# Performance work log

Hardware: AMD Instinct MI355X
Metric: run time of the kernel (lower is better)

The kernel has to match this reference:

```python
import jax, jax.numpy as jnp
import numpy as np

B, C, H, W_SP = 8, 2048, 28, 28   # last_conv feature map (ResNet-50, layer4 stride=1, 448px input)
D = 8192                          # count-sketch / CBP output dim
NUM_CLS = 200
L2_EPS = 1e-12                    # F.normalize default eps


def setup_inputs() -> dict:
    key = jax.random.key(0)
    ks = jax.random.split(key, 7)
    x = jax.random.normal(ks[0], (B, C, H, W_SP), dtype=jnp.float32)
    h1 = jax.random.randint(ks[1], (C,), 0, D, dtype=jnp.int32)
    h2 = jax.random.randint(ks[2], (C,), 0, D, dtype=jnp.int32)
    # Rademacher signs (count-sketch s vectors); map {0,1} -> {-1,+1}
    s1 = (2.0 * jax.random.bernoulli(ks[3], 0.5, (C,)).astype(jnp.float32) - 1.0)
    s2 = (2.0 * jax.random.bernoulli(ks[4], 0.5, (C,)).astype(jnp.float32) - 1.0)
    W_cls = jax.random.normal(ks[5], (D, NUM_CLS), dtype=jnp.float32) * 0.01
    b_cls = jnp.zeros((NUM_CLS,), dtype=jnp.float32)
    return {"x": x, "s1": s1, "s2": s2, "W_cls": W_cls, "b_cls": b_cls, "h1": h1, "h2": h2}


def _cbp_sum(xf, s1, s2, h1, h2):
    # xf: [B, L, C] per-pixel features.  Count-sketch each pixel twice, convolve
    # via FFT, then sum over all L spatial locations (== the original HxW loop).
    Bb, L, Cc = xf.shape
    sk1 = jnp.zeros((Bb, L, D), xf.dtype).at[..., h1].add(xf * s1)  # scatter-add over channels
    sk2 = jnp.zeros((Bb, L, D), xf.dtype).at[..., h2].add(xf * s2)
    f1 = jnp.fft.rfft(sk1, axis=-1)
    f2 = jnp.fft.rfft(sk2, axis=-1)
    y = jnp.fft.irfft(f1 * f2, n=D, axis=-1)  # [B, L, D] circular conv of sketches
    return y.sum(axis=1)                      # sum over spatial locations -> [B, D]


def reference(x, s1, s2, W_cls, b_cls, h1, h2):
    Bb, Cc, Hh, Ww = x.shape
    xf = x.transpose(0, 2, 3, 1).reshape(Bb, Hh * Ww, Cc)          # [B, L, C]
    y = _cbp_sum(xf, s1, s2, h1, h2)                               # [B, D]
    feat = jnp.sign(y) * jnp.sqrt(jnp.abs(y))                      # signed sqrt
    feat = feat / jnp.maximum(jnp.linalg.norm(feat, axis=1, keepdims=True), L2_EPS)
    logit = feat @ W_cls + b_cls
    return logit, feat
```

## Files before the change

kernel.cpp:

```cpp
#include <hip/hip_runtime.h>
#include <hip/hip_bf16.h>

#define BATCH 8
#define CH    2048
#define LSP   784
#define KPAD  832
#define KSTAGE 13
#define DDIM  8192
#define NCLS  200
#define NTILE 16
#define NGRID 512
#define NUNIT 1024
#define NSLOT 64
#define FXINV (1.0f/8192.0f)

typedef _Float16 f16x8 __attribute__((ext_vector_type(8)));
typedef float    f32x4 __attribute__((ext_vector_type(4)));

#define FATOMIC(p, v) unsafeAtomicAdd((p), (v))

__global__ __launch_bounds__(256) void split_kernel(
    const float* __restrict__ x,
    _Float16* __restrict__ xh,
    float* __restrict__ part, float* __restrict__ norm,
    const float* __restrict__ s1, const int* __restrict__ h1,
    const float* __restrict__ s2, const int* __restrict__ h2,
    float4* __restrict__ metaG,
    const float* __restrict__ bc, float* __restrict__ out,
    int exclusive)
{
    int idx = blockIdx.x * 256 + threadIdx.x;
    if (!exclusive && idx < NSLOT * BATCH * DDIM / 4)
        *(float4*)&part[idx * 4] = make_float4(0.f, 0.f, 0.f, 0.f);
    if (idx < CH)
        metaG[idx] = make_float4(s1[idx] * 64.0f, __int_as_float(h1[idx]),
                                 s2[idx] * 128.0f, __int_as_float(h2[idx]));
    if (idx < BATCH) norm[idx] = 0.0f;
    if (idx < BATCH * NCLS) out[idx] = bc[idx % NCLS];
    if (idx >= BATCH * CH * KPAD / 8) return;
    int v  = idx * 8;
    int bc_ = v / KPAD;
    int l  = v - bc_ * KPAD;
    f16x8 hv = {0, 0, 0, 0, 0, 0, 0, 0};
    if (l < LSP) {
        const float* xp = &x[(size_t)bc_ * LSP + l];
        float4 a = *(const float4*)xp;
        float4 c = *(const float4*)(xp + 4);
        hv[0] = (_Float16)a.x; hv[1] = (_Float16)a.y;
        hv[2] = (_Float16)a.z; hv[3] = (_Float16)a.w;
        hv[4] = (_Float16)c.x; hv[5] = (_Float16)c.y;
        hv[6] = (_Float16)c.z; hv[7] = (_Float16)c.w;
    }
    *(f16x8*)&xh[v] = hv;
}

__device__ __forceinline__ void stage64(
    const _Float16* __restrict__ src,
    unsigned short* lds,
    int wv, int lane, int s)
{
    const int rowi = lane >> 3;
    const int gc   = (lane & 7) ^ rowi;
    const _Float16* g0 = src + (size_t)rowi * KPAD + s * 64 + gc * 8;
#pragma unroll
    for (int q = 0; q < 4; ++q) {
        const int r0 = wv * 32 + q * 8;
        __builtin_amdgcn_global_load_lds(
            (__attribute__((address_space(1))) void*)(g0 + (size_t)r0 * KPAD),
            (__attribute__((address_space(3))) void*)(lds + r0 * 64),
            16, 0, 0);
    }
}

__global__ __launch_bounds__(256, 2) void gram_scatter_kernel(
    const _Float16* __restrict__ xh,
    const float4* __restrict__ metaG,
    float* __restrict__ part,
    int exclusive)
{
    __shared__ __align__(16) unsigned short smA[128 * 64];
    __shared__ __align__(16) unsigned short smB[128 * 64];
    __shared__ __align__(16) int bins[DDIM];

    const int tid  = threadIdx.x;
    const int lane = tid & 63;
    const int wv   = tid >> 6;
    const int bid  = blockIdx.x;
    const int b    = bid & 7;

    for (int i = tid; i < DDIM; i += 256) bins[i] = 0;

    const int wrow = (wv >> 1) * 64;
    const int wcol = (wv & 1) * 64;
    const int rsel = lane & 15;
    const int khi  = lane >> 4;

#pragma unroll 1
    for (int jj = 0; jj < 2; ++jj) {
        const int unit = bid + jj * NGRID;
        int npair, tMs[2], tNs[2];
        if (unit < 64) {
            const int t2 = (unit >> 3) * 2;
            npair = 2;
            tMs[0] = tNs[0] = t2;
            tMs[1] = tNs[1] = t2 + 1;
        } else {
            npair = 1;
            int i = (unit - 64) >> 3;
            int tM = 0, tN = 0;
#pragma unroll 1
            for (int t = 0; t < NTILE - 1; ++t) {
                int c = NTILE - 1 - t;
                if (i < c) { tM = t; tN = t + 1 + i; break; }
                i -= c;
            }
            tMs[0] = tM; tNs[0] = tN;
        }

#pragma unroll 1
        for (int pp = 0; pp < npair; ++pp) {
            const int tM = tMs[pp], tN = tNs[pp];
            const bool diag = (tM == tN);

            const _Float16* srcA = xh + ((size_t)b * CH + (size_t)tM * 128) * KPAD;
            const _Float16* srcB = xh + ((size_t)b * CH + (size_t)tN * 128) * KPAD;
            const unsigned short* fragB = diag ? smA : smB;

            f32x4 acc[4][4];
            const f32x4 zv = {0.0f, 0.0f, 0.0f, 0.0f};
#pragma unroll
            for (int mi = 0; mi < 4; ++mi)
#pragma unroll
                for (int ni = 0; ni < 4; ++ni) acc[mi][ni] = zv;

#pragma unroll 1
            for (int s = 0; s < KSTAGE; ++s) {
                stage64(srcA, smA, wv, lane, s);
                if (!diag) stage64(srcB, smB, wv, lane, s);
                __syncthreads();
#pragma unroll
                for (int t = 0; t < 2; ++t) {
                    const int co = ((((t << 2) + khi) ^ (rsel & 7)) << 3);
                    f16x8 ah[4], bh[4];
#pragma unroll
                    for (int i = 0; i < 4; ++i) {
                        ah[i] = *(const f16x8*)&smA[(wrow + i * 16 + rsel) * 64 + co];
                        bh[i] = *(const f16x8*)&fragB[(wcol + i * 16 + rsel) * 64 + co];
                    }
#pragma unroll
                    for (int mi = 0; mi < 4; ++mi)
#pragma unroll
                        for (int ni = 0; ni < 4; ++ni)
                            acc[mi][ni] = __builtin_amdgcn_mfma_f32_16x16x32_f16(
                                ah[mi], bh[ni], acc[mi][ni], 0, 0, 0);
                }
                __syncthreads();
            }

            const int c2b = tN * 128 + wcol + rsel;
            int   h1c[4], h2c[4]; float s1c[4], s2c[4];
#pragma unroll
            for (int ni = 0; ni < 4; ++ni) {
                float4 cm = metaG[c2b + ni * 16];
                s1c[ni] = cm.x; h1c[ni] = __float_as_int(cm.y);
                s2c[ni] = cm.z; h2c[ni] = __float_as_int(cm.w);
            }

            const int rowbase = tM * 128 + wrow + (khi << 2);
#pragma unroll
            for (int mi = 0; mi < 4; ++mi) {
                float4 rm[4];
#pragma unroll
                for (int r = 0; r < 4; ++r) rm[r] = metaG[rowbase + mi * 16 + r];
#pragma unroll
                for (int r = 0; r < 4; ++r) {
                    const float s1r = rm[r].x, s2r = rm[r].z;
                    const int h1r = __float_as_int(rm[r].y);
                    const int h2r = __float_as_int(rm[r].w);
#pragma unroll
                    for (int ni = 0; ni < 4; ++ni) {
                        float g = acc[mi][ni][r];
                        atomicAdd(&bins[(h1r + h2c[ni]) & (DDIM - 1)],
                                  (int)(s1r * s2c[ni] * g));
                        if (!diag)
                            atomicAdd(&bins[(h1c[ni] + h2r) & (DDIM - 1)],
                                      (int)(s1c[ni] * s2r * g));
                    }
                }
            }
        }
    }

    __syncthreads();

    if (exclusive) {
        float* pbase = part + ((size_t)((bid >> 3) * BATCH + b) * DDIM);
#pragma unroll 4
        for (int i = tid; i < DDIM / 4; i += 256) {
            int4 v = *(const int4*)&bins[i * 4];
            float4 f = make_float4((float)v.x * FXINV, (float)v.y * FXINV,
                                   (float)v.z * FXINV, (float)v.w * FXINV);
            *(float4*)&pbase[i * 4] = f;
        }
    } else {
        float* pbase = part + ((size_t)((bid >> 3) * BATCH + b) * DDIM);
        const int rot = (bid & 31) << 8;
        for (int i = tid; i < DDIM; i += 256) {
            int j = (i + rot) & (DDIM - 1);
            int v = bins[j];
            if (v != 0) FATOMIC(&pbase[j], (float)v * FXINV);
        }
    }
}

__global__ __launch_bounds__(256) void reduce_kernel(
    const float* __restrict__ part, float* __restrict__ y,
    float* __restrict__ norm)
{
    const int tid = threadIdx.x;
    const int b   = blockIdx.x & 7;
    const int d0  = (blockIdx.x >> 3) * 256 + tid;
    float s = 0.0f;
#pragma unroll 8
    for (int p = 0; p < NSLOT; ++p)
        s += part[((size_t)p * BATCH + b) * DDIM + d0];
    y[(size_t)b * DDIM + d0] = s;
    float ab = fabsf(s);
    __shared__ float red[256];
    red[tid] = ab;
    __syncthreads();
    for (int st = 128; st > 0; st >>= 1) {
        if (tid < st) red[tid] += red[tid + st];
        __syncthreads();
    }
    if (tid == 0) FATOMIC(&norm[b], red[0]);
}

__global__ __launch_bounds__(256) void logit_kernel(
    const float* __restrict__ y, const float* __restrict__ norm,
    const float* __restrict__ W, float* __restrict__ out)
{
    const int j = blockIdx.x;
    const int tid = threadIdx.x;
    __shared__ float fs[BATCH][64];
    __shared__ float inv[BATCH];
    if (tid < BATCH) inv[tid] = 1.0f / fmaxf(sqrtf(norm[tid]), 1e-12f);
    __syncthreads();
    for (int i = tid; i < BATCH * 64; i += 256) {
        int bb = i >> 6, dd = i & 63;
        float v = y[(size_t)bb * DDIM + j * 64 + dd];
        float f = copysignf(sqrtf(fabsf(v)), v) * inv[bb];
        fs[bb][dd] = f;
        out[BATCH * NCLS + (size_t)bb * DDIM + j * 64 + dd] = f;
    }
    __syncthreads();
    if (tid < NCLS) {
        float a[BATCH];
#pragma unroll
        for (int bb = 0; bb < BATCH; ++bb) a[bb] = 0.0f;
        for (int dd = 0; dd < 64; ++dd) {
            float w = W[(size_t)(j * 64 + dd) * NCLS + tid];
#pragma unroll
            for (int bb = 0; bb < BATCH; ++bb) a[bb] += fs[bb][dd] * w;
        }
#pragma unroll
        for (int bb = 0; bb < BATCH; ++bb)
            FATOMIC(&out[bb * NCLS + tid], a[bb]);
    }
}

extern "C" void kernel_launch(void* const* d_in, const int* in_sizes, int n_in,
                              void* d_out, int out_size, void* d_ws, size_t ws_size,
                              hipStream_t stream)
{
    const float* x  = (const float*)d_in[0];
    const float* s1 = (const float*)d_in[1];
    const float* s2 = (const float*)d_in[2];
    const float* W  = (const float*)d_in[3];
    const float* bc = (const float*)d_in[4];
    const int*   h1 = (const int*)d_in[5];
    const int*   h2 = (const int*)d_in[6];
    float* out = (float*)d_out;

    const size_t ybytes  = (size_t)BATCH * DDIM * sizeof(float);
    const size_t xhbytes = (size_t)BATCH * CH * KPAD * sizeof(_Float16);
    const size_t partbytes = (size_t)NSLOT * BATCH * DDIM * sizeof(float);

    const int exclusive = (ws_size >= partbytes + ybytes + 128 + xhbytes);

    char* ws = (char*)d_ws;
    float* part = (float*)ws;
    float* y    = (float*)(ws + partbytes);
    float4* metaG = (float4*)(ws + partbytes);
    float* norm = (float*)(ws + partbytes + ybytes);
    _Float16* xh = (_Float16*)(ws + partbytes + ybytes + 128);

    split_kernel<<<(BATCH * CH * KPAD / 8 + 255) / 256, 256, 0, stream>>>(
        x, xh, part, norm, s1, h1, s2, h2, metaG, bc, out, exclusive);

    gram_scatter_kernel<<<NGRID, 256, 0, stream>>>(
        xh, metaG, part, exclusive);

    reduce_kernel<<<256, 256, 0, stream>>>(part, y, norm);

    logit_kernel<<<128, 256, 0, stream>>>(y, norm, W, out);
}
```

Measured before the change: 162.1 us.

## Double-buffer gram tile staging and halve grid to four units per block

The Gram-matrix kernel now double-buffers the LDS A/B tiles. It prefetches the next K-stage, or the first stage of the next tile pair, with async global-to-LDS loads and uses a partial vmcnt wait instead of full syncthreads. The grid is halved so each block processes four units, and the partial-sum slot count shrinks to match. The goal is to hide global load latency behind MFMA work and cut the number of partial buffers to reduce. The cost is doubled LDS per block (occupancy likely drops to one block per CU, and the launch-bounds occupancy hint is removed) and fewer blocks to spread across CUs.

```diff
diff --git a/kernel.cpp b/kernel.cpp
--- a/kernel.cpp
+++ b/kernel.cpp
@@ -9,9 +9,9 @@
 #define DDIM  8192
 #define NCLS  200
 #define NTILE 16
-#define NGRID 512
+#define NGRID 256
 #define NUNIT 1024
-#define NSLOT 64
+#define NSLOT 32
 #define FXINV (1.0f/8192.0f)
 
 typedef _Float16 f16x8 __attribute__((ext_vector_type(8)));
@@ -72,14 +72,14 @@
     }
 }
 
-__global__ __launch_bounds__(256, 2) void gram_scatter_kernel(
+__global__ __launch_bounds__(256) void gram_scatter_kernel(
     const _Float16* __restrict__ xh,
     const float4* __restrict__ metaG,
     float* __restrict__ part,
     int exclusive)
 {
-    __shared__ __align__(16) unsigned short smA[128 * 64];
-    __shared__ __align__(16) unsigned short smB[128 * 64];
+    __shared__ __align__(16) unsigned short smA[2][128 * 64];
+    __shared__ __align__(16) unsigned short smB[2][128 * 64];
     __shared__ __align__(16) int bins[DDIM];
 
     const int tid  = threadIdx.x;
@@ -90,22 +90,15 @@
 
     for (int i = tid; i < DDIM; i += 256) bins[i] = 0;
 
-    const int wrow = (wv >> 1) * 64;
-    const int wcol = (wv & 1) * 64;
-    const int rsel = lane & 15;
-    const int khi  = lane >> 4;
-
+    int npairs = 0, tMl[5], tNl[5];
 #pragma unroll 1
-    for (int jj = 0; jj < 2; ++jj) {
+    for (int jj = 0; jj < 4; ++jj) {
         const int unit = bid + jj * NGRID;
-        int npair, tMs[2], tNs[2];
         if (unit < 64) {
             const int t2 = (unit >> 3) * 2;
-            npair = 2;
-            tMs[0] = tNs[0] = t2;
-            tMs[1] = tNs[1] = t2 + 1;
+            tMl[npairs] = tNl[npairs] = t2;     ++npairs;
+            tMl[npairs] = tNl[npairs] = t2 + 1; ++npairs;
         } else {
-            npair = 1;
             int i = (unit - 64) >> 3;
             int tM = 0, tN = 0;
 #pragma unroll 1
@@ -114,78 +107,116 @@
                 if (i < c) { tM = t; tN = t + 1 + i; break; }
                 i -= c;
             }
-            tMs[0] = tM; tNs[0] = tN;
-        }
+            tMl[npairs] = tM; tNl[npairs] = tN; ++npairs;
+        }
+    }
+
+    const int wrow = (wv >> 1) * 64;
+    const int wcol = (wv & 1) * 64;
+    const int rsel = lane & 15;
+    const int khi  = lane >> 4;
+
+    {
+        const _Float16* a0 = xh + ((size_t)b * CH + (size_t)tMl[0] * 128) * KPAD;
+        stage64(a0, smA[0], wv, lane, 0);
+        if (tMl[0] != tNl[0]) {
+            const _Float16* b0 = xh + ((size_t)b * CH + (size_t)tNl[0] * 128) * KPAD;
+            stage64(b0, smB[0], wv, lane, 0);
+        }
+    }
+
+    int g = 0;
 
 #pragma unroll 1
-        for (int pp = 0; pp < npair; ++pp) {
-            const int tM = tMs[pp], tN = tNs[pp];
-            const bool diag = (tM == tN);
-
-            const _Float16* srcA = xh + ((size_t)b * CH + (size_t)tM * 128) * KPAD;
-            const _Float16* srcB = xh + ((size_t)b * CH + (size_t)tN * 128) * KPAD;
-            const unsigned short* fragB = diag ? smA : smB;
-
-            f32x4 acc[4][4];
-            const f32x4 zv = {0.0f, 0.0f, 0.0f, 0.0f};
-#pragma unroll
-            for (int mi = 0; mi < 4; ++mi)
-#pragma unroll
-                for (int ni = 0; ni < 4; ++ni) acc[mi][ni] = zv;
+    for (int p = 0; p < npairs; ++p) {
+        const int tM = tMl[p], tN = tNl[p];
+        const bool diag = (tM == tN);
+
+        const _Float16* srcA = xh + ((size_t)b * CH + (size_t)tM * 128) * KPAD;
+        const _Float16* srcB = xh + ((size_t)b * CH + (size_t)tN * 128) * KPAD;
+
+        f32x4 acc[4][4];
+        const f32x4 zv = {0.0f, 0.0f, 0.0f, 0.0f};
+#pragma unroll
+        for (int mi = 0; mi < 4; ++mi)
+#pragma unroll
+            for (int ni = 0; ni < 4; ++ni) acc[mi][ni] = zv;
 
 #pragma unroll 1
-            for (int s = 0; s < KSTAGE; ++s) {
-                stage64(srcA, smA, wv, lane, s);
-                if (!diag) stage64(srcB, smB, wv, lane, s);
-                __syncthreads();
-#pragma unroll
-                for (int t = 0; t < 2; ++t) {
-                    const int co = ((((t << 2) + khi) ^ (rsel & 7)) << 3);
-                    f16x8 ah[4], bh[4];
-#pragma unroll
-                    for (int i = 0; i < 4; ++i) {
-                        ah[i] = *(const f16x8*)&smA[(wrow + i * 16 + rsel) * 64 + co];
-                        bh[i] = *(const f16x8*)&fragB[(wcol + i * 16 + rsel) * 64 + co];
-                    }
-#pragma unroll
-                    for (int mi = 0; mi < 4; ++mi)
-#pragma unroll
-                        for (int ni = 0; ni < 4; ++ni)
-                            acc[mi][ni] = __builtin_amdgcn_mfma_f32_16x16x32_f16(
-                                ah[mi], bh[ni], acc[mi][ni], 0, 0, 0);
+        for (int s = 0; s < KSTAGE; ++s) {
+            const int curb = g & 1, nxtb = curb ^ 1;
+            int k = 0;
+            if (s + 1 < KSTAGE) {
+                stage64(srcA, smA[nxtb], wv, lane, s + 1);
+                if (!diag) { stage64(srcB, smB[nxtb], wv, lane, s + 1); k = 8; }
+                else k = 4;
+            } else if (p + 1 < npairs) {
+                const int nM = tMl[p + 1], nN = tNl[p + 1];
+                const _Float16* nA = xh + ((size_t)b * CH + (size_t)nM * 128) * KPAD;
+                stage64(nA, smA[nxtb], wv, lane, 0);
+                if (nM != nN) {
+                    const _Float16* nB = xh + ((size_t)b * CH + (size_t)nN * 128) * KPAD;
+                    stage64(nB, smB[nxtb], wv, lane, 0);
+                    k = 8;
+                } else k = 4;
+            }
+            __builtin_amdgcn_sched_barrier(0);
+            if (k == 8)      asm volatile("s_waitcnt vmcnt(8)" ::: "memory");
+            else if (k == 4) asm volatile("s_waitcnt vmcnt(4)" ::: "memory");
+            else             asm volatile("s_waitcnt vmcnt(0)" ::: "memory");
+            __builtin_amdgcn_s_barrier();
+            __builtin_amdgcn_sched_barrier(0);
+
+            const unsigned short* bufA = smA[curb];
+            const unsigned short* bufB = diag ? smA[curb] : smB[curb];
+#pragma unroll
+            for (int t = 0; t < 2; ++t) {
+                const int co = ((((t << 2) + khi) ^ (rsel & 7)) << 3);
+                f16x8 ah[4], bh[4];
+#pragma unroll
+                for (int i = 0; i < 4; ++i) {
+                    ah[i] = *(const f16x8*)&bufA[(wrow + i * 16 + rsel) * 64 + co];
+                    bh[i] = *(const f16x8*)&bufB[(wcol + i * 16 + rsel) * 64 + co];
                 }
-                __syncthreads();
+#pragma unroll
+                for (int mi = 0; mi < 4; ++mi)
+#pragma unroll
+                    for (int ni = 0; ni < 4; ++ni)
+                        acc[mi][ni] = __builtin_amdgcn_mfma_f32_16x16x32_f16(
+                            ah[mi], bh[ni], acc[mi][ni], 0, 0, 0);
             }
-
-            const int c2b = tN * 128 + wcol + rsel;
-            int   h1c[4], h2c[4]; float s1c[4], s2c[4];
-#pragma unroll
-            for (int ni = 0; ni < 4; ++ni) {
-                float4 cm = metaG[c2b + ni * 16];
-                s1c[ni] = cm.x; h1c[ni] = __float_as_int(cm.y);
-                s2c[ni] = cm.z; h2c[ni] = __float_as_int(cm.w);
-            }
-
-            const int rowbase = tM * 128 + wrow + (khi << 2);
-#pragma unroll
-            for (int mi = 0; mi < 4; ++mi) {
-                float4 rm[4];
-#pragma unroll
-                for (int r = 0; r < 4; ++r) rm[r] = metaG[rowbase + mi * 16 + r];
-#pragma unroll
-                for (int r = 0; r < 4; ++r) {
-                    const float s1r = rm[r].x, s2r = rm[r].z;
-                    const int h1r = __float_as_int(rm[r].y);
-                    const int h2r = __float_as_int(rm[r].w);
-#pragma unroll
-                    for (int ni = 0; ni < 4; ++ni) {
-                        float g = acc[mi][ni][r];
-                        atomicAdd(&bins[(h1r + h2c[ni]) & (DDIM - 1)],
-                                  (int)(s1r * s2c[ni] * g));
-                        if (!diag)
-                            atomicAdd(&bins[(h1c[ni] + h2r) & (DDIM - 1)],
-                                      (int)(s1c[ni] * s2r * g));
-                    }
+            __builtin_amdgcn_sched_barrier(0);
+            __builtin_amdgcn_s_barrier();
+            ++g;
+        }
+
+        const int c2b = tN * 128 + wcol + rsel;
+        int   h1c[4], h2c[4]; float s1c[4], s2c[4];
+#pragma unroll
+        for (int ni = 0; ni < 4; ++ni) {
+            float4 cm = metaG[c2b + ni * 16];
+            s1c[ni] = cm.x; h1c[ni] = __float_as_int(cm.y);
+            s2c[ni] = cm.z; h2c[ni] = __float_as_int(cm.w);
+        }
+        const int rowbase = tM * 128 + wrow + (khi << 2);
+#pragma unroll
+        for (int mi = 0; mi < 4; ++mi) {
+            float4 rm[4];
+#pragma unroll
+            for (int r = 0; r < 4; ++r) rm[r] = metaG[rowbase + mi * 16 + r];
+#pragma unroll
+            for (int r = 0; r < 4; ++r) {
+                const float s1r = rm[r].x, s2r = rm[r].z;
+                const int h1r = __float_as_int(rm[r].y);
+                const int h2r = __float_as_int(rm[r].w);
+#pragma unroll
+                for (int ni = 0; ni < 4; ++ni) {
+                    float g2 = acc[mi][ni][r];
+                    atomicAdd(&bins[(h1r + h2c[ni]) & (DDIM - 1)],
+                              (int)(s1r * s2c[ni] * g2));
+                    if (!diag)
+                        atomicAdd(&bins[(h1c[ni] + h2r) & (DDIM - 1)],
+                                  (int)(s1c[ni] * s2r * g2));
                 }
             }
         }
```

Result: slower. 185.3 us (+14.4%).
